# Kernel tuning notes

Measured on AMD Instinct MI355X. Metric: run time of the kernel, lower is better.

The kernel has to match this reference:

```python
import jax, jax.numpy as jnp
import numpy as np

B, T, E, H2, V, NT = 256, 192, 300, 256, 11626, 13  # batch, max_len, embed, hidden_dim, vocab, num_tags
START, STOP = 0, 10
NEG = -10000.0


def setup_inputs() -> dict:
    key = jax.random.key(0)
    ks = jax.random.split(key, 13)
    H = H2 // 2
    s = 0.1
    trans = jax.random.normal(ks[12], (NT, NT), dtype=jnp.float32)
    trans = trans.at[START, :].set(NEG).at[:, STOP].set(NEG)
    return {
        "sentence": jax.random.randint(ks[0], (B, T), 0, V),
        "seq_len": jax.random.randint(ks[1], (B,), 1, T + 1),  # lengths >= 1
        "tags": jax.random.randint(ks[2], (B, T), 0, 10),
        "embedding": jax.random.normal(ks[3], (V, E), dtype=jnp.float32) * s,
        "W_ih_f": jax.random.normal(ks[4], (4 * H, E), dtype=jnp.float32) * s,
        "W_hh_f": jax.random.normal(ks[5], (4 * H, H), dtype=jnp.float32) * s,
        "b_f": jnp.zeros((4 * H,), jnp.float32),
        "W_ih_b": jax.random.normal(ks[6], (4 * H, E), dtype=jnp.float32) * s,
        "W_hh_b": jax.random.normal(ks[7], (4 * H, H), dtype=jnp.float32) * s,
        "b_b": jnp.zeros((4 * H,), jnp.float32),
        "W_fc": jax.random.normal(ks[8], (NT, H2), dtype=jnp.float32) * s,
        "b_fc": jnp.zeros((NT,), jnp.float32),
        "transitions": trans,
    }


def _rev_within_len(x, lens):
    # reverse each sequence's first `len` positions (mimics packed-sequence reverse dir)
    t = jnp.arange(x.shape[1])
    idx = jnp.where(t[None, :] < lens[:, None], lens[:, None] - 1 - t[None, :], t[None, :])
    return jnp.take_along_axis(x, idx[:, :, None], axis=1)


def _lstm_dir(x, lens, W_ih, W_hh, b):
    # x: [B,T,E] -> [B,T,H]; PyTorch gate order i,f,g,o; padded steps frozen + zeroed output
    Bx, Tx, _ = x.shape
    H = W_hh.shape[1]
    mask = (jnp.arange(Tx)[None, :] < lens[:, None]).astype(x.dtype)  # [B,T]
    gx = jnp.einsum('bte,ge->btg', x, W_ih) + b  # precompute input projections

    def step(carry, inp):
        h, c = carry
        g_x, m = inp  # [B,4H], [B,1]
        g = g_x + h @ W_hh.T
        i, f, gg, o = jnp.split(g, 4, axis=-1)
        c_new = jax.nn.sigmoid(f) * c + jax.nn.sigmoid(i) * jnp.tanh(gg)
        h_new = jax.nn.sigmoid(o) * jnp.tanh(c_new)
        h = jnp.where(m > 0, h_new, h)
        c = jnp.where(m > 0, c_new, c)
        return (h, c), h * m

    h0 = jnp.zeros((Bx, H), x.dtype)
    _, hs = jax.lax.scan(step, (h0, h0), (gx.transpose(1, 0, 2), mask.T[:, :, None]))
    return hs.transpose(1, 0, 2)


def _crf_nll(feats, tags, transitions):
    # feats: [B,T,NT]; iterate over ALL T padded positions (faithful to source)
    def fwd_step(alpha, feat):
        # alpha_new[b,j] = logsumexp_i(alpha[b,i] + trans[j,i]) + feat[b,j]
        nxt = jax.nn.logsumexp(alpha[:, None, :] + transitions[None, :, :], axis=-1) + feat
        return nxt, None

    alpha0 = jnp.full((feats.shape[0], NT), NEG, feats.dtype).at[:, START].set(0.0)
    alphaT, _ = jax.lax.scan(fwd_step, alpha0, feats.transpose(1, 0, 2))
    fwd_score = jax.nn.logsumexp(alphaT + transitions[STOP][None, :], axis=-1)  # [B]

    tags_ext = jnp.concatenate([jnp.full((feats.shape[0], 1), START, tags.dtype), tags], axis=1)
    trans_sc = transitions[tags_ext[:, 1:], tags_ext[:, :-1]].sum(-1)
    emit_sc = jnp.take_along_axis(feats, tags[:, :, None], axis=2)[:, :, 0].sum(-1)
    gold = trans_sc + emit_sc + transitions[STOP, tags[:, -1]]
    return fwd_score - gold  # [B]


def reference(sentence, seq_len, tags, embedding, W_ih_f, W_hh_f, b_f,
              W_ih_b, W_hh_b, b_b, W_fc, b_fc, transitions):
    lens = jnp.clip(seq_len, 1, T)  # seq_len.clamp(max=192)
    emb = embedding[sentence]  # [B,T,E]
    h_f = _lstm_dir(emb, lens, W_ih_f, W_hh_f, b_f)
    h_b = _rev_within_len(_lstm_dir(_rev_within_len(emb, lens), lens, W_ih_b, W_hh_b, b_b), lens)
    out = jnp.concatenate([h_f, h_b], axis=-1)  # [B,T,H2]
    feats = jnp.einsum('bth,gh->btg', out, W_fc) + b_fc  # [B,T,NT]
    nll = _crf_nll(feats, tags, transitions)
    return nll.mean()
```

## Files before the change

kernel.cpp:

```cpp
#include <hip/hip_runtime.h>
#include <hip/hip_bf16.h>


#define B_   256
#define T_   192
#define E_   300
#define KP   320
#define V_   11626
#define H_   128
#define G4   512
#define NG   1024
#define NT_  13
#define NEGV -10000.0f
#define HSTR 144

typedef __attribute__((ext_vector_type(8))) short bf16x8;
typedef __attribute__((ext_vector_type(4))) float f32x4;
typedef __attribute__((ext_vector_type(4))) unsigned short u16x4;

__device__ __forceinline__ unsigned short f2bf(float f) {
    return (unsigned short)(__float_as_uint(f) >> 16);
}
__device__ __forceinline__ float bf2f(unsigned short h) {
    return __uint_as_float(((unsigned)h) << 16);
}
__device__ __forceinline__ float sigf(float x) {
    return __builtin_amdgcn_rcpf(1.0f + __expf(-x));
}
__device__ __forceinline__ float tanhfast(float x) {
    return __builtin_amdgcn_rcpf(1.0f + __expf(-2.0f * x)) * 2.0f - 1.0f;
}
__device__ __forceinline__ void barrier_lgkm() {
    asm volatile("s_waitcnt lgkmcnt(0)\n\ts_barrier" ::: "memory");
}

__global__ void pack_kernel(const float* __restrict__ Wf, const float* __restrict__ Wb,
                            const float* __restrict__ Whf, const float* __restrict__ Whb,
                            const float* __restrict__ emb,
                            const int* __restrict__ seq_len,
                            unsigned short* __restrict__ Wp, unsigned short* __restrict__ Whp,
                            unsigned short* __restrict__ Ep, int* __restrict__ prefix,
                            float* __restrict__ out) {
    int blk = blockIdx.x;
    int k = threadIdx.x;
    if (blk == 0) {
        __shared__ int sc[257];
        if (k == 0) { sc[0] = 0; out[0] = 0.0f; }
        if (k < 256) sc[k + 1] = min(max(seq_len[k], 1), T_);
        __syncthreads();
        #pragma unroll 1
        for (int off = 1; off < 257; off <<= 1) {
            int v = (k >= off && k < 257) ? sc[k - off] : 0;
            __syncthreads();
            if (k < 257) sc[k] += v;
            __syncthreads();
        }
        if (k < 257) prefix[k] = sc[k];
    }
    if (blk < NG) {
        float v = 0.0f;
        if (k < E_) v = (blk < G4) ? Wf[blk * E_ + k] : Wb[(blk - G4) * E_ + k];
        Wp[blk * KP + k] = f2bf(v);
    } else if (blk < NG + 1024) {
        int t = blk - NG;
        int d = t >> 9, g = t & 511;
        if (k < H_) {
            const float* src = d ? Whb : Whf;
            float v = src[g * H_ + k];
            int w = (g >> 4) & 7, j = g >> 7, colq = g & 15;
            int kc = k >> 5, quad = (k >> 3) & 3, e = k & 7;
            Whp[((((size_t)(d * 8 + w) * 4 + j) * 4 + kc) * 64 + quad * 16 + colq) * 8 + e] = f2bf(v);
        }
    } else {
        int r = blk - NG - 1024;
        float v = (k < E_) ? emb[(size_t)r * E_ + k] : 0.0f;
        Ep[(size_t)r * KP + k] = f2bf(v);
    }
}

__global__ __launch_bounds__(256, 3) void gemm_kernel(const unsigned short* __restrict__ Ep,
                                                      const int* __restrict__ sent,
                                                      const unsigned short* __restrict__ Bw,
                                                      const float* __restrict__ bF,
                                                      const float* __restrict__ bB,
                                                      const int* __restrict__ prefix,
                                                      unsigned short* __restrict__ C) {
    __shared__ __align__(16) unsigned short As[128 * 64];
    __shared__ __align__(16) unsigned short Bs[128 * 64];
    __shared__ int pfx[257];
    const int tid  = threadIdx.x;
    for (int i = tid; i < 257; i += 256) pfx[i] = prefix[i];
    __syncthreads();
    const int sumL = pfx[256];
    const int mBase = blockIdx.y * 128;
    if (mBase >= sumL) return;
    const int lane = tid & 63;
    const int wave = tid >> 6;
    const int wr = wave >> 1, wc = wave & 1;
    const int colL = lane & 15;
    const int bx = blockIdx.x;
    const int d  = bx >> 2;
    const int w0 = (bx & 3) * 2;
    int toks[4];
    #pragma unroll
    for (int j = 0; j < 4; j++) {
        int ci = mBase + ((tid + 256 * j) >> 3);
        ci = min(ci, sumL - 1);
        int lo = 0, hi = 256;
        #pragma unroll
        for (int it = 0; it < 8; it++) {
            int mid = (lo + hi) >> 1;
            if (pfx[mid] <= ci) lo = mid; else hi = mid;
        }
        toks[j] = sent[lo * T_ + (ci - pfx[lo])];
    }
    f32x4 acc[4][4] = {};
    for (int k0 = 0; k0 < KP; k0 += 64) {
        #pragma unroll
        for (int j = 0; j < 4; j++) {
            int c   = tid + 256 * j;
            int col = (c & 7) * 8;
            __builtin_amdgcn_global_load_lds(
                (const void*)(Ep + (size_t)toks[j] * KP + k0 + col),
                (void*)((char*)As + c * 16), 16, 0, 0);
            int row = c >> 3;
            int ws = row >> 6, jj = (row >> 4) & 3, cc = row & 15;
            int srcrow = d * 512 + (8 * jj + w0 + ws) * 16 + cc;
            __builtin_amdgcn_global_load_lds(
                (const void*)(Bw + (size_t)srcrow * KP + k0 + col),
                (void*)((char*)Bs + c * 16), 16, 0, 0);
        }
        __syncthreads();
        #pragma unroll
        for (int ks = 0; ks < 2; ks++) {
            bf16x8 af[4], bfr[4];
            #pragma unroll
            for (int i = 0; i < 4; i++) {
                int arow = wr * 64 + i * 16 + colL;
                af[i]  = *(const bf16x8*)(As + arow * 64 + ks * 32 + (lane >> 4) * 8);
                int brow = wc * 64 + i * 16 + colL;
                bfr[i] = *(const bf16x8*)(Bs + brow * 64 + ks * 32 + (lane >> 4) * 8);
            }
            #pragma unroll
            for (int i = 0; i < 4; i++)
                #pragma unroll
                for (int n2 = 0; n2 < 4; n2++)
                    acc[i][n2] = __builtin_amdgcn_mfma_f32_16x16x32_bf16(af[i], bfr[n2], acc[i][n2], 0, 0, 0);
        }
        __syncthreads();
    }
    const float* bias_d = d ? bB : bF;
    float bj[4];
    #pragma unroll
    for (int n2 = 0; n2 < 4; n2++) bj[n2] = bias_d[(8 * n2 + w0 + wc) * 16 + colL];
    #pragma unroll
    for (int i = 0; i < 4; i++)
        #pragma unroll
        for (int r = 0; r < 4; r++) {
            int row = mBase + wr * 64 + i * 16 + (lane >> 4) * 4 + r;
            if (row < sumL) {
                u16x4 v;
                #pragma unroll
                for (int n2 = 0; n2 < 4; n2++) v[n2] = f2bf(acc[i][n2][r] + bj[n2]);
                *(u16x4*)(C + (size_t)row * NG + d * 512 + (w0 + wc) * 64 + colL * 4) = v;
            }
        }
}

__global__ __launch_bounds__(576, 1) void lstm_kernel(const unsigned short* __restrict__ gxP,
                                                      const unsigned short* __restrict__ Whp,
                                                      const int* __restrict__ seq_len,
                                                      const int* __restrict__ prefix,
                                                      const float* __restrict__ Wfc,
                                                      float* __restrict__ featsF,
                                                      float* __restrict__ featsB) {
    __shared__ __align__(16) unsigned short hL[2][16 * HSTR];
    __shared__ int Ls[4];
    __shared__ int Ps[4];
    __shared__ int maxLs;
    const int tid  = threadIdx.x;
    const int wave = tid >> 6;
    const int lane = tid & 63;
    const int col  = lane & 15;
    const int quad = lane >> 4;
    const int dir  = blockIdx.x & 1;
    const int b0   = (blockIdx.x >> 1) * 4;
    float* fOut = dir ? featsB : featsF;

    if (tid < 4) {
        Ls[tid] = min(max(seq_len[b0 + tid], 1), T_);
        Ps[tid] = prefix[b0 + tid];
    }
    __syncthreads();
    if (tid == 0) { int m = 0; for (int i = 0; i < 4; i++) m = max(m, Ls[i]); maxLs = m; }
    __syncthreads();
    const int maxL = maxLs;
    const int Lq = Ls[quad];
    const int dNG = dir ? -NG : NG;

    bf16x8 Bf[4][4];
    bf16x8 Wf8[4];
    const unsigned short* rb = nullptr;
    int ofs2 = 0;
    u16x4 gx0v = {}, gx1v = {};
    float* fb = nullptr;
    int foff = 0;

    if (wave < 8) {
        #pragma unroll
        for (int j = 0; j < 4; j++)
            #pragma unroll
            for (int kc = 0; kc < 4; kc++)
                Bf[j][kc] = *(const bf16x8*)(Whp +
                    ((((size_t)(dir * 8 + wave) * 4 + j) * 4 + kc) * 64 + lane) * 8);
        int p0 = dir ? (Lq - 1) : 0;
        rb = gxP + ((size_t)(Ps[quad] + p0)) * NG + dir * 512 + wave * 64 + col * 4;
        gx0v = *(const u16x4*)(rb);
        gx1v = *(const u16x4*)(rb + ((Lq > 1) ? dNG : 0));
        ofs2 = min(2, Lq - 1) * dNG;
    } else {
        #pragma unroll
        for (int kc = 0; kc < 4; kc++)
            #pragma unroll
            for (int e = 0; e < 8; e++) {
                float v = (col < NT_) ? Wfc[col * 256 + dir * H_ + kc * 32 + quad * 8 + e] : 0.0f;
                Wf8[kc][e] = (short)f2bf(v);
            }
        fb = fOut + (size_t)(b0 + quad) * T_ * NT_ + col;
        foff = (dir ? (Lq - 1) : 0) * NT_;
    }
    const int fd = dir ? -NT_ : NT_;

    float cst = 0.0f;
    bf16x8 Af[4];
    #pragma unroll
    for (int kc = 0; kc < 4; kc++)
        #pragma unroll
        for (int e = 0; e < 8; e++) Af[kc][e] = 0;

    auto step_body = [&](int s, u16x4& gxs, int par) {
        if (wave < 8) {
            f32x4 acc[4];
            #pragma unroll
            for (int j = 0; j < 4; j++) {
                acc[j][0] = bf2f(gxs[j]);
                acc[j][1] = 0.f; acc[j][2] = 0.f; acc[j][3] = 0.f;
            }
            gxs = *(const u16x4*)(rb + ofs2);
            ofs2 = (s + 3 < Lq) ? ofs2 + dNG : ofs2;
            #pragma unroll
            for (int kc = 0; kc < 4; kc++)
                #pragma unroll
                for (int j = 0; j < 4; j++)
                    acc[j] = __builtin_amdgcn_mfma_f32_16x16x32_bf16(Af[kc], Bf[j][kc], acc[j], 0, 0, 0);
            float cn = sigf(acc[1][0]) * cst + sigf(acc[0][0]) * tanhfast(acc[2][0]);
            cst = cn;
            float hn = sigf(acc[3][0]) * tanhfast(cn);
            hL[par][(quad * 4) * HSTR + wave * 16 + col] = f2bf(hn);
        }
        barrier_lgkm();
        #pragma unroll
        for (int kc = 0; kc < 4; kc++)
            Af[kc] = *(const bf16x8*)(&hL[par][col * HSTR + kc * 32 + quad * 8]);
        if (wave == 8) {
            f32x4 fc = (f32x4){0.f, 0.f, 0.f, 0.f};
            #pragma unroll
            for (int kc = 0; kc < 4; kc++)
                fc = __builtin_amdgcn_mfma_f32_16x16x32_bf16(Af[kc], Wf8[kc], fc, 0, 0, 0);
            if (col < NT_ && s < Lq) fb[foff] = fc[0];
            foff += fd;
        }
    };

    for (int s = 0; s < maxL; s += 2) {
        step_body(s, gx0v, 0);
        if (s + 1 < maxL) step_body(s + 1, gx1v, 1);
    }
}

__global__ __launch_bounds__(64) void crf_kernel(const float* __restrict__ fF,
                                                 const float* __restrict__ fB,
                                                 const float* __restrict__ bfc,
                                                 const float* __restrict__ trans,
                                                 const int* __restrict__ tags,
                                                 const int* __restrict__ seq_len,
                                                 float* __restrict__ out) {
    __shared__ __align__(16) float feat_lds[2 * 208];
    __shared__ float Tlds[NT_ * NT_];
    const int lane = threadIdx.x;
    const int b = blockIdx.x;
    const int Lb = min(max(seq_len[b], 1), T_);
    const float* fFb = fF + (size_t)b * T_ * NT_;
    const float* fBb = fB + (size_t)b * T_ * NT_;
    const int* tg = tags + (size_t)b * T_;

    for (int i = lane; i < NT_ * NT_; i += 64) Tlds[i] = trans[i];

    const int jc = min(lane, NT_ - 1);
    float Tj[NT_];
    #pragma unroll
    for (int i = 0; i < NT_; i++) Tj[i] = trans[jc * NT_ + i];
    const float bj  = bfc[jc];
    const float T10 = trans[10 * NT_ + jc];
    float alj = (jc == 0 && lane == 0) ? 0.0f : NEGV;

    const int e0 = lane * 4;
    const bool ldact = (lane < 52);
    float4 vF = {}, vB = {};
    if (ldact) { vF = *(const float4*)(fFb + e0); vB = *(const float4*)(fBb + e0); }

    #pragma unroll 1
    for (int c = 0; c < 12; ++c) {
        if (ldact) {
            float4 w;
            #pragma unroll
            for (int k = 0; k < 4; k++) {
                unsigned g = (unsigned)(c * 208 + e0 + k);
                unsigned t = g / 13u;
                float s = ((const float*)&vF)[k] + ((const float*)&vB)[k];
                ((float*)&w)[k] = (t < (unsigned)Lb) ? s : 0.0f;
            }
            *(float4*)&feat_lds[(c & 1) * 208 + e0] = w;
            if (c < 11) {
                vF = *(const float4*)(fFb + (c + 1) * 208 + e0);
                vB = *(const float4*)(fBb + (c + 1) * 208 + e0);
            }
        }
        barrier_lgkm();
        const int fbase = (c & 1) * 208;
        for (int tt = 0; tt < 16; ++tt) {
            float a0  = __shfl(alj, 0, 64),  a1  = __shfl(alj, 1, 64);
            float a2  = __shfl(alj, 2, 64),  a3  = __shfl(alj, 3, 64);
            float a4  = __shfl(alj, 4, 64),  a5  = __shfl(alj, 5, 64);
            float a6  = __shfl(alj, 6, 64),  a7  = __shfl(alj, 7, 64);
            float a8  = __shfl(alj, 8, 64),  a9  = __shfl(alj, 9, 64);
            float a10 = __shfl(alj, 10, 64), a11 = __shfl(alj, 11, 64);
            float a12 = __shfl(alj, 12, 64);
            float feat = feat_lds[fbase + tt * NT_ + jc];
            float v0 = a0 + Tj[0],  v1 = a1 + Tj[1],  v2 = a2 + Tj[2],  v3 = a3 + Tj[3];
            float v4 = a4 + Tj[4],  v5 = a5 + Tj[5],  v6 = a6 + Tj[6],  v7 = a7 + Tj[7];
            float v8 = a8 + Tj[8],  v9 = a9 + Tj[9],  v10 = a10 + Tj[10], v11 = a11 + Tj[11];
            float v12 = a12 + Tj[12];
            float p0 = fmaxf(v0, v1), p1 = fmaxf(v2, v3), p2 = fmaxf(v4, v5);
            float p3 = fmaxf(v6, v7), p4 = fmaxf(v8, v9), p5 = fmaxf(v10, v11);
            float q0 = fmaxf(p0, p1), q1 = fmaxf(p2, p3), q2 = fmaxf(p4, p5);
            float m = fmaxf(fmaxf(q0, q1), fmaxf(q2, v12));
            float e0_ = __expf(v0 - m),  e1_ = __expf(v1 - m),  e2_ = __expf(v2 - m);
            float e3_ = __expf(v3 - m),  e4_ = __expf(v4 - m),  e5_ = __expf(v5 - m);
            float e6_ = __expf(v6 - m),  e7_ = __expf(v7 - m),  e8_ = __expf(v8 - m);
            float e9_ = __expf(v9 - m),  e10_ = __expf(v10 - m), e11_ = __expf(v11 - m);
            float e12_ = __expf(v12 - m);
            float s0 = e0_ + e1_, s1 = e2_ + e3_, s2 = e4_ + e5_, s3 = e6_ + e7_;
            float s4 = e8_ + e9_, s5 = e10_ + e11_;
            float u0 = s0 + s1, u1 = s2 + s3, u2 = s4 + s5;
            float ss = (u0 + u1) + (u2 + e12_);
            alj = m + __logf(ss) + feat + bj;
        }
    }

    float gp = 0.0f;
    #pragma unroll
    for (int u = 0; u < 3; ++u) {
        int t = lane + u * 64;
        int tt_ = tg[t];
        int pv = (t == 0) ? 0 : tg[t - 1];
        float e = bfc[tt_];
        if (t < Lb) e += fFb[t * NT_ + tt_] + fBb[t * NT_ + tt_];
        gp += Tlds[tt_ * NT_ + pv] + e;
    }
    #pragma unroll
    for (int o = 32; o > 0; o >>= 1) gp += __shfl_down(gp, o, 64);

    float vj = (lane < NT_) ? (alj + T10) : -3.0e38f;
    float mm = vj;
    #pragma unroll
    for (int o = 32; o > 0; o >>= 1) mm = fmaxf(mm, __shfl_down(mm, o, 64));
    mm = __shfl(mm, 0, 64);
    float se = (lane < NT_) ? __expf(vj - mm) : 0.0f;
    #pragma unroll
    for (int o = 32; o > 0; o >>= 1) se += __shfl_down(se, o, 64);
    if (lane == 0) {
        float fwd = mm + __logf(se);
        float gold = gp + Tlds[10 * NT_ + tg[T_ - 1]];
        atomicAdd(out, (fwd - gold) * (1.0f / 256.0f));
    }
}

extern "C" void kernel_launch(void* const* d_in, const int* in_sizes, int n_in,
                              void* d_out, int out_size, void* d_ws, size_t ws_size,
                              hipStream_t stream) {
    const int*   sentence  = (const int*)d_in[0];
    const int*   seq_len   = (const int*)d_in[1];
    const int*   tags      = (const int*)d_in[2];
    const float* embedding = (const float*)d_in[3];
    const float* W_ih_f    = (const float*)d_in[4];
    const float* W_hh_f    = (const float*)d_in[5];
    const float* b_f       = (const float*)d_in[6];
    const float* W_ih_b    = (const float*)d_in[7];
    const float* W_hh_b    = (const float*)d_in[8];
    const float* b_b       = (const float*)d_in[9];
    const float* W_fc      = (const float*)d_in[10];
    const float* b_fc      = (const float*)d_in[11];
    const float* trans     = (const float*)d_in[12];
    float* out = (float*)d_out;

    char* ws = (char*)d_ws;
    const size_t M = (size_t)B_ * T_;
    unsigned short* Wp  = (unsigned short*)(ws);
    unsigned short* Ep  = (unsigned short*)(ws + 655360);
    unsigned short* gx  = (unsigned short*)(ws + 8096000);
    float* featsF = (float*)(ws + 108759296);
    float* featsB = (float*)(ws + 111315200);
    unsigned short* Whp = (unsigned short*)(ws + 113871104);
    int* prefix = (int*)(ws + 114133248);

    pack_kernel<<<NG + 1024 + V_, KP, 0, stream>>>(W_ih_f, W_ih_b, W_hh_f, W_hh_b,
                                                   embedding, seq_len, Wp, Whp, Ep, prefix, out);
    dim3 gg(8, (int)(M / 128));
    gemm_kernel<<<gg, 256, 0, stream>>>(Ep, sentence, Wp, b_f, b_b, prefix, gx);
    lstm_kernel<<<128, 576, 0, stream>>>(gx, Whp, seq_len, prefix, W_fc, featsF, featsB);
    crf_kernel<<<B_, 64, 0, stream>>>(featsF, featsB, b_fc, trans, tags, seq_len, out);
}
```

Before: 289.8 us.

## Fuse input-projection GEMM and LSTM into one kernel with atomic-counter handoff

```diff
diff --git a/kernel.cpp b/kernel.cpp
--- a/kernel.cpp
+++ b/kernel.cpp
@@ -39,14 +39,28 @@
                             const float* __restrict__ emb,
                             const int* __restrict__ seq_len,
                             unsigned short* __restrict__ Wp, unsigned short* __restrict__ Whp,
-                            unsigned short* __restrict__ Ep, int* __restrict__ prefix,
+                            unsigned short* __restrict__ Ep,
+                            int* __restrict__ perm, int* __restrict__ pfxs,
+                            int* __restrict__ cnt,
                             float* __restrict__ out) {
     int blk = blockIdx.x;
     int k = threadIdx.x;
     if (blk == 0) {
+        __shared__ int Lsm[256];
         __shared__ int sc[257];
-        if (k == 0) { sc[0] = 0; out[0] = 0.0f; }
-        if (k < 256) sc[k + 1] = min(max(seq_len[k], 1), T_);
+        if (k == 0) { out[0] = 0.0f; sc[0] = 0; }
+        if (k < 256) Lsm[k] = min(max(seq_len[k], 1), T_);
+        for (int i = k; i < 384; i += 320) cnt[i] = 0;
+        __syncthreads();
+        if (k < 256) {
+            int L = Lsm[k]; int r = 0;
+            for (int b = 0; b < 256; ++b) {
+                int Lb = Lsm[b];
+                r += (Lb > L) || (Lb == L && b < k);
+            }
+            perm[r] = k;
+            sc[r + 1] = L;
+        }
         __syncthreads();
         #pragma unroll 1
         for (int off = 1; off < 257; off <<= 1) {
@@ -55,7 +69,7 @@
             if (k < 257) sc[k] += v;
             __syncthreads();
         }
-        if (k < 257) prefix[k] = sc[k];
+        if (k < 257) pfxs[k] = sc[k];
     }
     if (blk < NG) {
         float v = 0.0f;
@@ -78,203 +92,246 @@
     }
 }
 
-__global__ __launch_bounds__(256, 3) void gemm_kernel(const unsigned short* __restrict__ Ep,
-                                                      const int* __restrict__ sent,
-                                                      const unsigned short* __restrict__ Bw,
-                                                      const float* __restrict__ bF,
-                                                      const float* __restrict__ bB,
-                                                      const int* __restrict__ prefix,
-                                                      unsigned short* __restrict__ C) {
-    __shared__ __align__(16) unsigned short As[128 * 64];
-    __shared__ __align__(16) unsigned short Bs[128 * 64];
-    __shared__ int pfx[257];
-    const int tid  = threadIdx.x;
-    for (int i = tid; i < 257; i += 256) pfx[i] = prefix[i];
-    __syncthreads();
-    const int sumL = pfx[256];
-    const int mBase = blockIdx.y * 128;
-    if (mBase >= sumL) return;
-    const int lane = tid & 63;
-    const int wave = tid >> 6;
-    const int wr = wave >> 1, wc = wave & 1;
-    const int colL = lane & 15;
-    const int bx = blockIdx.x;
-    const int d  = bx >> 2;
-    const int w0 = (bx & 3) * 2;
-    int toks[4];
-    #pragma unroll
-    for (int j = 0; j < 4; j++) {
-        int ci = mBase + ((tid + 256 * j) >> 3);
-        ci = min(ci, sumL - 1);
-        int lo = 0, hi = 256;
-        #pragma unroll
-        for (int it = 0; it < 8; it++) {
-            int mid = (lo + hi) >> 1;
-            if (pfx[mid] <= ci) lo = mid; else hi = mid;
-        }
-        toks[j] = sent[lo * T_ + (ci - pfx[lo])];
-    }
-    f32x4 acc[4][4] = {};
-    for (int k0 = 0; k0 < KP; k0 += 64) {
-        #pragma unroll
-        for (int j = 0; j < 4; j++) {
-            int c   = tid + 256 * j;
-            int col = (c & 7) * 8;
-            __builtin_amdgcn_global_load_lds(
-                (const void*)(Ep + (size_t)toks[j] * KP + k0 + col),
-                (void*)((char*)As + c * 16), 16, 0, 0);
-            int row = c >> 3;
-            int ws = row >> 6, jj = (row >> 4) & 3, cc = row & 15;
-            int srcrow = d * 512 + (8 * jj + w0 + ws) * 16 + cc;
-            __builtin_amdgcn_global_load_lds(
-                (const void*)(Bw + (size_t)srcrow * KP + k0 + col),
-                (void*)((char*)Bs + c * 16), 16, 0, 0);
-        }
-        __syncthreads();
-        #pragma unroll
-        for (int ks = 0; ks < 2; ks++) {
-            bf16x8 af[4], bfr[4];
+__global__ __launch_bounds__(576, 2) void fused_kernel(
+        const unsigned short* __restrict__ Ep, const int* __restrict__ sent,
+        const unsigned short* __restrict__ Bw, const float* __restrict__ bF,
+        const float* __restrict__ bB, const int* __restrict__ perm,
+        const int* __restrict__ pfxs, int* __restrict__ cnt,
+        unsigned short* __restrict__ gxP, const unsigned short* __restrict__ Whp,
+        const int* __restrict__ seq_len, const float* __restrict__ Wfc,
+        float* __restrict__ featsF, float* __restrict__ featsB) {
+
+    __shared__ __align__(16) union SMU {
+        struct {
+            unsigned short As[128 * 64];
+            unsigned short Bs[256 * 64];
+            int pfx[257];
+            int prm[256];
+        } g;
+        struct {
+            unsigned short hL[2][16 * HSTR];
+            int Ls[4]; int Ps[4]; int Rw[4]; int maxLs;
+        } l;
+    } sm;
+
+    const int bid = blockIdx.x;
+    const int tid = threadIdx.x;
+
+    if (bid < 128) {
+        for (int i = tid; i < 257; i += 576) sm.g.pfx[i] = pfxs[i];
+        for (int i = tid; i < 256; i += 576) sm.g.prm[i] = perm[i];
+        __syncthreads();
+        const int sumL = sm.g.pfx[256];
+        const int Y  = (sumL + 127) >> 7;
+        const int TT = Y * 4;
+        const int nIter = (TT + 127) >> 7;
+        const int lane = tid & 63;
+        const int wave = tid >> 6;
+        const int act = (tid < 512);
+        const int wr = wave >> 2, wc = wave & 3;
+        const int colL = lane & 15;
+
+        for (int it = 0; it < nIter; ++it) {
+            const int u = it * 128 + bid;
+            const int valid = act && (u < TT);
+            const int y = u >> 2, bx = u & 3;
+            const int mBase = y * 128;
+            const int d = bx >> 1, w0p = (bx & 1) * 4;
+            int toks[2] = {0, 0};
+            if (valid) {
+                #pragma unroll
+                for (int ja = 0; ja < 2; ja++) {
+                    int ci = mBase + ((tid + 512 * ja) >> 3);
+                    ci = min(ci, sumL - 1);
+                    int lo = 0, hi = 256;
+                    #pragma unroll
+                    for (int itb = 0; itb < 8; itb++) {
+                        int mid = (lo + hi) >> 1;
+                        if (sm.g.pfx[mid] <= ci) lo = mid; else hi = mid;
+                    }
+                    toks[ja] = sent[sm.g.prm[lo] * T_ + (ci - sm.g.pfx[lo])];
+                }
+            }
+            f32x4 acc[4][4] = {};
+            for (int k0 = 0; k0 < KP; k0 += 64) {
+                if (valid) {
+                    #pragma unroll
+                    for (int ja = 0; ja < 2; ja++) {
+                        int c = tid + 512 * ja;
+                        int col = (c & 7) * 8;
+                        __builtin_amdgcn_global_load_lds(
+                            (const void*)(Ep + (size_t)toks[ja] * KP + k0 + col),
+                            (void*)((char*)sm.g.As + c * 16), 16, 0, 0);
+                    }
+                    #pragma unroll
+                    for (int jb = 0; jb < 4; jb++) {
+                        int c = tid + 512 * jb;
+                        int col = (c & 7) * 8;
+                        int row = c >> 3;
+                        int ws = row >> 6, jj = (row >> 4) & 3, cc = row & 15;
+                        int srcrow = d * 512 + (8 * jj + w0p + ws) * 16 + cc;
+                        __builtin_amdgcn_global_load_lds(
+                            (const void*)(Bw + (size_t)srcrow * KP + k0 + col),
+                            (void*)((char*)sm.g.Bs + c * 16), 16, 0, 0);
+                    }
+                }
+                __syncthreads();
+                if (valid) {
+                    #pragma unroll
+                    for (int ks = 0; ks < 2; ks++) {
+                        bf16x8 af[4], bfr[4];
+                        #pragma unroll
+                        for (int i = 0; i < 4; i++) {
+                            int arow = wr * 64 + i * 16 + colL;
+                            af[i]  = *(const bf16x8*)(sm.g.As + arow * 64 + ks * 32 + (lane >> 4) * 8);
+                            int brow = wc * 64 + i * 16 + colL;
+                            bfr[i] = *(const bf16x8*)(sm.g.Bs + brow * 64 + ks * 32 + (lane >> 4) * 8);
+                        }
+                        #pragma unroll
+                        for (int i = 0; i < 4; i++)
+                            #pragma unroll
+                            for (int n2 = 0; n2 < 4; n2++)
+                                acc[i][n2] = __builtin_amdgcn_mfma_f32_16x16x32_bf16(af[i], bfr[n2], acc[i][n2], 0, 0, 0);
+                    }
+                }
+                __syncthreads();
+            }
+            if (valid) {
+                const float* bias_d = d ? bB : bF;
+                float bj[4];
+                #pragma unroll
+                for (int n2 = 0; n2 < 4; n2++) bj[n2] = bias_d[(8 * n2 + w0p + wc) * 16 + colL];
+                #pragma unroll
+                for (int i = 0; i < 4; i++)
+                    #pragma unroll
+                    for (int r = 0; r < 4; r++) {
+                        int row = mBase + wr * 64 + i * 16 + (lane >> 4) * 4 + r;
+                        if (row < sumL) {
+                            u16x4 v;
+                            #pragma unroll
+                            for (int n2 = 0; n2 < 4; n2++) v[n2] = f2bf(acc[i][n2][r] + bj[n2]);
+                            *(u16x4*)(gxP + (size_t)row * NG + d * 512 + (w0p + wc) * 64 + colL * 4) = v;
+                        }
+                    }
+            }
+            __threadfence();
+            __syncthreads();
+            if (u < TT && tid == 0)
+                __hip_atomic_fetch_add(&cnt[y], 1, __ATOMIC_RELEASE, __HIP_MEMORY_SCOPE_AGENT);
+        }
+    } else {
+        const int lidx = bid - 128;
+        const int g   = lidx >> 1;
+        const int dir = lidx & 1;
+        float* fOut = dir ? featsB : featsF;
+
+        if (tid == 0) {
+            const int need = pfxs[4 * g + 4];
+            const int Yg = (need + 127) >> 7;
+            for (int y = 0; y < Yg; ++y) {
+                while (__hip_atomic_load(&cnt[y], __ATOMIC_RELAXED, __HIP_MEMORY_SCOPE_AGENT) < 4)
+                    __builtin_amdgcn_s_sleep(8);
+            }
+            (void)__hip_atomic_load(&cnt[0], __ATOMIC_ACQUIRE, __HIP_MEMORY_SCOPE_AGENT);
+        }
+        __syncthreads();
+
+        const int wave = tid >> 6;
+        const int lane = tid & 63;
+        const int col  = lane & 15;
+        const int quad = lane >> 4;
+
+        if (tid < 4) {
+            int row = perm[4 * g + tid];
+            sm.l.Rw[tid] = row;
+            sm.l.Ls[tid] = min(max(seq_len[row], 1), T_);
+            sm.l.Ps[tid] = pfxs[4 * g + tid];
+        }
+        __syncthreads();
+        if (tid == 0) { int m = 0; for (int i = 0; i < 4; i++) m = max(m, sm.l.Ls[i]); sm.l.maxLs = m; }
+        __syncthreads();
+        const int maxL = sm.l.maxLs;
+        const int Lq = sm.l.Ls[quad];
+        const int dNG = dir ? -NG : NG;
+
+        bf16x8 Bf[4][4];
+        bf16x8 Wf8[4];
+        const unsigned short* rb = nullptr;
+        int ofs2 = 0;
+        u16x4 gx0v = {}, gx1v = {};
+        float* fb = nullptr;
+        int foff = 0;
+
+        if (wave < 8) {
             #pragma unroll
-            for (int i = 0; i < 4; i++) {
-                int arow = wr * 64 + i * 16 + colL;
-                af[i]  = *(const bf16x8*)(As + arow * 64 + ks * 32 + (lane >> 4) * 8);
-                int brow = wc * 64 + i * 16 + colL;
-                bfr[i] = *(const bf16x8*)(Bs + brow * 64 + ks * 32 + (lane >> 4) * 8);
-            }
-            #pragma unroll
-            for (int i = 0; i < 4; i++)
-                #pragma unroll
-                for (int n2 = 0; n2 < 4; n2++)
-                    acc[i][n2] = __builtin_amdgcn_mfma_f32_16x16x32_bf16(af[i], bfr[n2], acc[i][n2], 0, 0, 0);
-        }
-        __syncthreads();
-    }
-    const float* bias_d = d ? bB : bF;
-    float bj[4];
-    #pragma unroll
-    for (int n2 = 0; n2 < 4; n2++) bj[n2] = bias_d[(8 * n2 + w0 + wc) * 16 + colL];
-    #pragma unroll
-    for (int i = 0; i < 4; i++)
-        #pragma unroll
-        for (int r = 0; r < 4; r++) {
-            int row = mBase + wr * 64 + i * 16 + (lane >> 4) * 4 + r;
-            if (row < sumL) {
-                u16x4 v;
-                #pragma unroll
-                for (int n2 = 0; n2 < 4; n2++) v[n2] = f2bf(acc[i][n2][r] + bj[n2]);
-                *(u16x4*)(C + (size_t)row * NG + d * 512 + (w0 + wc) * 64 + colL * 4) = v;
-            }
-        }
-}
-
-__global__ __launch_bounds__(576, 1) void lstm_kernel(const unsigned short* __restrict__ gxP,
-                                                      const unsigned short* __restrict__ Whp,
-                                                      const int* __restrict__ seq_len,
-                                                      const int* __restrict__ prefix,
-                                                      const float* __restrict__ Wfc,
-                                                      float* __restrict__ featsF,
-                                                      float* __restrict__ featsB) {
-    __shared__ __align__(16) unsigned short hL[2][16 * HSTR];
-    __shared__ int Ls[4];
-    __shared__ int Ps[4];
-    __shared__ int maxLs;
-    const int tid  = threadIdx.x;
-    const int wave = tid >> 6;
-    const int lane = tid & 63;
-    const int col  = lane & 15;
-    const int quad = lane >> 4;
-    const int dir  = blockIdx.x & 1;
-    const int b0   = (blockIdx.x >> 1) * 4;
-    float* fOut = dir ? featsB : featsF;
-
-    if (tid < 4) {
-        Ls[tid] = min(max(seq_len[b0 + tid], 1), T_);
-        Ps[tid] = prefix[b0 + tid];
-    }
-    __syncthreads();
-    if (tid == 0) { int m = 0; for (int i = 0; i < 4; i++) m = max(m, Ls[i]); maxLs = m; }
-    __syncthreads();
-    const int maxL = maxLs;
-    const int Lq = Ls[quad];
-    const int dNG = dir ? -NG : NG;
-
-    bf16x8 Bf[4][4];
-    bf16x8 Wf8[4];
-    const unsigned short* rb = nullptr;
-    int ofs2 = 0;
-    u16x4 gx0v = {}, gx1v = {};
-    float* fb = nullptr;
-    int foff = 0;
-
-    if (wave < 8) {
-        #pragma unroll
-        for (int j = 0; j < 4; j++)
+            for (int j = 0; j < 4; j++)
+                #pragma unroll
+                for (int kc = 0; kc < 4; kc++)
+                    Bf[j][kc] = *(const bf16x8*)(Whp +
+                        ((((size_t)(dir * 8 + wave) * 4 + j) * 4 + kc) * 64 + lane) * 8);
+            int p0 = dir ? (Lq - 1) : 0;
+            rb = gxP + ((size_t)(sm.l.Ps[quad] + p0)) * NG + dir * 512 + wave * 64 + col * 4;
+            gx0v = *(const u16x4*)(rb);
+            gx1v = *(const u16x4*)(rb + ((Lq > 1) ? dNG : 0));
+            ofs2 = min(2, Lq - 1) * dNG;
+        } else {
             #pragma unroll
             for (int kc = 0; kc < 4; kc++)
-                Bf[j][kc] = *(const bf16x8*)(Whp +
-                    ((((size_t)(dir * 8 + wave) * 4 + j) * 4 + kc) * 64 + lane) * 8);
-        int p0 = dir ? (Lq - 1) : 0;
-        rb = gxP + ((size_t)(Ps[quad] + p0)) * NG + dir * 512 + wave * 64 + col * 4;
-        gx0v = *(const u16x4*)(rb);
-        gx1v = *(const u16x4*)(rb + ((Lq > 1) ? dNG : 0));
-        ofs2 = min(2, Lq - 1) * dNG;
-    } else {
+                #pragma unroll
+                for (int e = 0; e < 8; e++) {
+                    float v = (col < NT_) ? Wfc[col * 256 + dir * H_ + kc * 32 + quad * 8 + e] : 0.0f;
+                    Wf8[kc][e] = (short)f2bf(v);
+                }
+            fb = fOut + (size_t)sm.l.Rw[quad] * T_ * NT_ + col;
+            foff = (dir ? (Lq - 1) : 0) * NT_;
+        }
+        const int fd = dir ? -NT_ : NT_;
+
+        float cst = 0.0f;
+        bf16x8 Af[4];
         #pragma unroll
         for (int kc = 0; kc < 4; kc++)
             #pragma unroll
-            for (int e = 0; e < 8; e++) {
-                float v = (col < NT_) ? Wfc[col * 256 + dir * H_ + kc * 32 + quad * 8 + e] : 0.0f;
-                Wf8[kc][e] = (short)f2bf(v);
-            }
-        fb = fOut + (size_t)(b0 + quad) * T_ * NT_ + col;
-        foff = (dir ? (Lq - 1) : 0) * NT_;
-    }
-    const int fd = dir ? -NT_ : NT_;
-
-    float cst = 0.0f;
-    bf16x8 Af[4];
-    #pragma unroll
-    for (int kc = 0; kc < 4; kc++)
-        #pragma unroll
-        for (int e = 0; e < 8; e++) Af[kc][e] = 0;
-
-    auto step_body = [&](int s, u16x4& gxs, int par) {
-        if (wave < 8) {
-            f32x4 acc[4];
-            #pragma unroll
-            for (int j = 0; j < 4; j++) {
-                acc[j][0] = bf2f(gxs[j]);
-                acc[j][1] = 0.f; acc[j][2] = 0.f; acc[j][3] = 0.f;
-            }
-            gxs = *(const u16x4*)(rb + ofs2);
-            ofs2 = (s + 3 < Lq) ? ofs2 + dNG : ofs2;
+            for (int e = 0; e < 8; e++) Af[kc][e] = 0;
+
+        auto step_body = [&](int s, u16x4& gxs, int par) {
+            if (wave < 8) {
+                f32x4 acc[4];
+                #pragma unroll
+                for (int j = 0; j < 4; j++) {
+                    acc[j][0] = bf2f(gxs[j]);
+                    acc[j][1] = 0.f; acc[j][2] = 0.f; acc[j][3] = 0.f;
+                }
+                gxs = *(const u16x4*)(rb + ofs2);
+                ofs2 = (s + 3 < Lq) ? ofs2 + dNG : ofs2;
+                #pragma unroll
+                for (int kc = 0; kc < 4; kc++)
+                    #pragma unroll
+                    for (int j = 0; j < 4; j++)
+                        acc[j] = __builtin_amdgcn_mfma_f32_16x16x32_bf16(Af[kc], Bf[j][kc], acc[j], 0, 0, 0);
+                float cn = sigf(acc[1][0]) * cst + sigf(acc[0][0]) * tanhfast(acc[2][0]);
+                cst = cn;
+                float hn = sigf(acc[3][0]) * tanhfast(cn);
+                sm.l.hL[par][(quad * 4) * HSTR + wave * 16 + col] = f2bf(hn);
+            }
+            barrier_lgkm();
             #pragma unroll
             for (int kc = 0; kc < 4; kc++)
-                #pragma unroll
-                for (int j = 0; j < 4; j++)
-                    acc[j] = __builtin_amdgcn_mfma_f32_16x16x32_bf16(Af[kc], Bf[j][kc], acc[j], 0, 0, 0);
-            float cn = sigf(acc[1][0]) * cst + sigf(acc[0][0]) * tanhfast(acc[2][0]);
-            cst = cn;
-            float hn = sigf(acc[3][0]) * tanhfast(cn);
-            hL[par][(quad * 4) * HSTR + wave * 16 + col] = f2bf(hn);
-        }
-        barrier_lgkm();
-        #pragma unroll
-        for (int kc = 0; kc < 4; kc++)
-            Af[kc] = *(const bf16x8*)(&hL[par][col * HSTR + kc * 32 + quad * 8]);
-        if (wave == 8) {
-            f32x4 fc = (f32x4){0.f, 0.f, 0.f, 0.f};
-            #pragma unroll
-            for (int kc = 0; kc < 4; kc++)
-                fc = __builtin_amdgcn_mfma_f32_16x16x32_bf16(Af[kc], Wf8[kc], fc, 0, 0, 0);
-            if (col < NT_ && s < Lq) fb[foff] = fc[0];
-            foff += fd;
-        }
-    };
-
-    for (int s = 0; s < maxL; s += 2) {
-        step_body(s, gx0v, 0);
-        if (s + 1 < maxL) step_body(s + 1, gx1v, 1);
+                Af[kc] = *(const bf16x8*)(&sm.l.hL[par][col * HSTR + kc * 32 + quad * 8]);
+            if (wave == 8) {
+                f32x4 fc = (f32x4){0.f, 0.f, 0.f, 0.f};
+                #pragma unroll
+                for (int kc = 0; kc < 4; kc++)
+                    fc = __builtin_amdgcn_mfma_f32_16x16x32_bf16(Af[kc], Wf8[kc], fc, 0, 0, 0);
+                if (col < NT_ && s < Lq) fb[foff] = fc[0];
+                foff += fd;
+            }
+        };
+
+        for (int s = 0; s < maxL; s += 2) {
+            step_body(s, gx0v, 0);
+            if (s + 1 < maxL) step_body(s + 1, gx1v, 1);
+        }
     }
 }
 
@@ -405,19 +462,21 @@
     float* out = (float*)d_out;
 
     char* ws = (char*)d_ws;
-    const size_t M = (size_t)B_ * T_;
     unsigned short* Wp  = (unsigned short*)(ws);
     unsigned short* Ep  = (unsigned short*)(ws + 655360);
     unsigned short* gx  = (unsigned short*)(ws + 8096000);
     float* featsF = (float*)(ws + 108759296);
     float* featsB = (float*)(ws + 111315200);
     unsigned short* Whp = (unsigned short*)(ws + 113871104);
-    int* prefix = (int*)(ws + 114133248);
+    int* perm = (int*)(ws + 114133248);
+    int* pfxs = (int*)(ws + 114134272);
+    int* cnt  = (int*)(ws + 114135312);
 
     pack_kernel<<<NG + 1024 + V_, KP, 0, stream>>>(W_ih_f, W_ih_b, W_hh_f, W_hh_b,
-                                                   embedding, seq_len, Wp, Whp, Ep, prefix, out);
-    dim3 gg(8, (int)(M / 128));
-    gemm_kernel<<<gg, 256, 0, stream>>>(Ep, sentence, Wp, b_f, b_b, prefix, gx);
-    lstm_kernel<<<128, 576, 0, stream>>>(gx, Whp, seq_len, prefix, W_fc, featsF, featsB);
+                                                   embedding, seq_len, Wp, Whp, Ep,
+                                                   perm, pfxs, cnt, out);
+    fused_kernel<<<256, 576, 0, stream>>>(Ep, sentence, Wp, b_f, b_b,
+                                          perm, pfxs, cnt, gx, Whp, seq_len,
+                                          W_fc, featsF, featsB);
     crf_kernel<<<B_, 64, 0, stream>>>(featsF, featsB, b_fc, trans, tags, seq_len, out);
 }
```

After: 513.5 us. 1.77x slower.
